# Optimization experiments

Measured on AMD Instinct MI355X. Metric: run time of the kernel, lower is better.

The kernel has to match this reference:

```python
import jax, jax.numpy as jnp
import numpy as np

# Faithful JAX port of RayObsGraph.forward with T=1.
# torch_geometric GraphConv(x, edge_index) with add-aggregation and no edge
# weights computes: out[i] = lin_root(x[i]) + lin_rel(sum_{(j->i) in E} x[j]),
# where lin_root has no bias and lin_rel has a bias. dense_to_sparse(adj)
# yields an edge (row j -> col i) for every nonzero adj[j, i], so the
# aggregation equals binarize(adj)^T @ x, computed batched here instead of the
# original per-sample Python loop.

GS = 128      # graph_size
OBS = 1024    # obs_dim
H = 256       # gcn_h_size
OUT = 1024    # gcn_outsize
NO = 18       # num_outputs
B = 256

def setup_inputs() -> dict:
    key = jax.random.key(0)
    ks = jax.random.split(key, 16)
    inp = {
        "flat": jax.random.normal(ks[0], (B, OBS), jnp.float32),
        "nodes": jax.random.normal(ks[1], (B, GS, OBS), jnp.float32),
        "num_nodes": jax.random.randint(ks[2], (B,), 0, GS),
        "adj": jax.random.randint(ks[3], (B, GS, GS), 0, 2),
        "seq_lens": jnp.ones((B,), jnp.int32),
        # GraphConv 0: lin_rel (bias) + lin_root (no bias)
        "W0_rel": jax.random.normal(ks[4], (OBS, H), jnp.float32) / np.sqrt(OBS),
        "b0": jnp.zeros((H,), jnp.float32),
        "W0_root": jax.random.normal(ks[5], (OBS, H), jnp.float32) / np.sqrt(OBS),
        # GraphConv 1
        "W1_rel": jax.random.normal(ks[6], (H, OUT), jnp.float32) / np.sqrt(H),
        "b1": jnp.zeros((OUT,), jnp.float32),
        "W1_root": jax.random.normal(ks[7], (H, OUT), jnp.float32) / np.sqrt(H),
        # logit / value branches (SlimFC, activation None)
        "Wl": jax.random.normal(ks[8], (OUT, NO), jnp.float32) / np.sqrt(OUT),
        "bl": jnp.zeros((NO,), jnp.float32),
        "Wv": jax.random.normal(ks[9], (OUT, 1), jnp.float32) / np.sqrt(OUT),
        "bv": jnp.zeros((1,), jnp.float32),
    }
    return inp

def _forward(flat, nodes, adj, num_nodes,
             W0_rel, b0, W0_root, W1_rel, b1, W1_root, Wl, bl, Wv, bv):
    bsz = flat.shape[0]
    bi = jnp.arange(bsz)
    n = num_nodes
    nm1 = jnp.maximum(n - 1, 0)
    has_prev = n > 0

    # dense_to_sparse treats any nonzero entry as an edge (weight unused)
    A = (adj != 0).astype(flat.dtype)                       # [B, GS, GS]
    A = A.at[bi, n, n].set(1.0)
    A = A.at[bi, n, nm1].set(jnp.where(has_prev, 1.0, A[bi, n, nm1]))
    A = A.at[bi, nm1, n].set(jnp.where(has_prev, 1.0, A[bi, nm1, n]))

    # write current observation into node slot num_nodes
    x = nodes.at[bi, n].set(flat)                           # [B, GS, OBS]

    At = jnp.swapaxes(A, 1, 2)                              # message j->i: A^T
    aggr0 = jnp.einsum('bij,bjd->bid', At, x)               # [B, GS, OBS]
    h0 = jax.nn.relu(aggr0 @ W0_rel + b0 + x @ W0_root)     # [B, GS, H]
    aggr1 = jnp.einsum('bij,bjd->bid', At, h0)              # [B, GS, H]
    h1 = jax.nn.relu(aggr1 @ W1_rel + b1 + h0 @ W1_root)    # [B, GS, OUT]

    node_out = h1[bi, n]                                    # [B, OUT]
    logits = node_out @ Wl + bl                             # [B, NO]
    values = (node_out @ Wv + bv).squeeze(-1)               # [B]
    return logits, values

def reference(flat, nodes, num_nodes, adj, seq_lens,
              W0_rel, b0, W0_root, W1_rel, b1, W1_root, Wl, bl, Wv, bv):
    # seq_lens only determines B = len(seq_lens); T = flat.shape[0] // B = 1
    del seq_lens
    return _forward(flat, nodes, adj, num_nodes,
                    W0_rel, b0, W0_root, W1_rel, b1, W1_root, Wl, bl, Wv, bv)
```

## Files before the change

### kernel.cpp

```cpp
#include <hip/hip_runtime.h>
#include <hip/hip_bf16.h>
#include <cstdint>
#include <cstddef>

#define GS     128
#define OBS    1024
#define HSZ    256
#define OUTSZ  1024
#define NOUT   18
#define BATCH  256

typedef short  short8  __attribute__((ext_vector_type(8)));
typedef float  f32x4   __attribute__((ext_vector_type(4)));

__device__ __forceinline__ uint32_t f2bf_bits(float f) {
  uint32_t u = __builtin_bit_cast(uint32_t, f);
  return (u + 0x7fffu + ((u >> 16) & 1u)) >> 16;
}
__device__ __forceinline__ float bf_bits2f(uint32_t b) {
  return __builtin_bit_cast(float, b << 16);
}
__device__ __forceinline__ uint4 cvt8s(const float4 a, const float4 b) {
  float v[8] = {a.x, a.y, a.z, a.w, b.x, b.y, b.z, b.w};
  uint32_t h[8];
#pragma unroll
  for (int e = 0; e < 8; ++e) h[e] = f2bf_bits(v[e]);
  return make_uint4(h[0] | (h[1] << 16), h[2] | (h[3] << 16),
                    h[4] | (h[5] << 16), h[6] | (h[7] << 16));
}

__global__ __launch_bounds__(256) void prep_kernel(
    const float* __restrict__ W0_rel, const float* __restrict__ W0_root,
    ushort* __restrict__ WtP, const float* __restrict__ Wl,
    const float* __restrict__ Wv, float* __restrict__ WlT,
    const float* __restrict__ W1_rel, const float* __restrict__ W1_root,
    ushort* __restrict__ W1bf)
{
  __shared__ float T[64][65];
  const int blk = blockIdx.x;
  const int t = threadIdx.x;
  if (blk < 128) {
    const int k0 = (blk & 15) * 64;
    const int n0 = (blk >> 4) * 64;
    for (int idx = t; idx < 4096; idx += 256) {
      const int r = idx >> 6, c = idx & 63;
      const int n = n0 + c;
      T[r][c] = (n < HSZ) ? W0_rel[(size_t)(k0 + r) * HSZ + n]
                          : W0_root[(size_t)(k0 + r) * HSZ + (n - HSZ)];
    }
    __syncthreads();
    for (int idx = t; idx < 4096; idx += 256) {
      const int r = idx >> 6, c = idx & 63;
      const int kk = k0 + c;
      WtP[((size_t)((kk >> 5) * 512 + n0 + r)) * 32 + (kk & 31)] =
          (ushort)f2bf_bits(T[c][r]);
    }
  } else if (blk < 132) {
    const int o = (blk - 128) * 256 + t;
#pragma unroll
    for (int c = 0; c < NOUT; ++c)
      WlT[(size_t)c * OUTSZ + o] = Wl[(size_t)o * NOUT + c];
    WlT[(size_t)18 * OUTSZ + o] = Wv[o];
  } else {
    const int base = (blk - 132) * 16384;
    for (int it = 0; it < 64; ++it) {
      const int idx = base + it * 256 + t;
      const int k = idx >> 10, o = idx & 1023;
      const float v = (k < HSZ) ? W1_rel[(size_t)k * OUTSZ + o]
                                : W1_root[(size_t)(k - HSZ) * OUTSZ + o];
      W1bf[idx] = (ushort)f2bf_bits(v);
    }
  }
}

__global__ __launch_bounds__(256, 1) void mega_kernel(
    const float* __restrict__ flat, const float* __restrict__ nodes,
    const int* __restrict__ num_nodes, const int* __restrict__ adj,
    const float* __restrict__ b0, const ushort* __restrict__ WtP,
    const ushort* __restrict__ W1bf, const float* __restrict__ b1,
    const float* __restrict__ WlT, const float* __restrict__ bl,
    const float* __restrict__ bv, float* __restrict__ out)
{
  __shared__ ushort   Ys[256][264];
  __shared__ ushort   As[128][40];
  __shared__ uint32_t rm[128][4];
  __shared__ uint32_t cmL[128][4];
  __shared__ float    a1s[256];
  __shared__ float    rns[256];
  __shared__ float    pl[19][4];

  const int b  = blockIdx.x;
  const int nb = num_nodes[b];
  const int t  = threadIdx.x;
  const int wv = t >> 6, lane = t & 63;
  const int ln = lane & 15, q = lane >> 4;

#pragma unroll 4
  for (int i = 0; i < 32; ++i) {
    const int k = wv * 32 + i;
    const int* arow = adj + ((size_t)b * GS + k) * GS;
    const unsigned long long m0 = __ballot(arow[lane] != 0);
    const unsigned long long m1 = __ballot(arow[64 + lane] != 0);
    if (lane == 0) {
      rm[k][0] = (uint32_t)m0; rm[k][1] = (uint32_t)(m0 >> 32);
      rm[k][2] = (uint32_t)m1; rm[k][3] = (uint32_t)(m1 >> 32);
    }
  }
  __syncthreads();
  if (t < 128) {
    uint32_t c0 = 0, c1 = 0, c2 = 0, c3 = 0;
    const int w = t >> 5, sh = t & 31;
#pragma unroll 8
    for (int k = 0; k < 128; ++k) {
      const uint32_t bit = (rm[k][w] >> sh) & 1u;
      if (k < 32)      c0 |= bit << k;
      else if (k < 64) c1 |= bit << (k - 32);
      else if (k < 96) c2 |= bit << (k - 64);
      else             c3 |= bit << (k - 96);
    }
    cmL[t][0] = c0; cmL[t][1] = c1; cmL[t][2] = c2; cmL[t][3] = c3;
  }
  __syncthreads();
  if (t == 0) {
    cmL[nb][nb >> 5] |= 1u << (nb & 31);
    if (nb > 0) {
      cmL[nb - 1][nb >> 5] |= 1u << (nb & 31);
      cmL[nb][(nb - 1) >> 5] |= 1u << ((nb - 1) & 31);
    }
  }

  const int arow2 = t >> 1;
  const int akb   = (t & 1) * 16;
  const float* xsrc = ((arow2 == nb) ? (flat + (size_t)b * OBS)
                                     : (nodes + ((size_t)b * GS + arow2) * OBS)) + akb;
  const ushort* bptr = WtP + ((size_t)(wv * 128 + ln)) * 32 + q * 8;

  f32x4 acc[8][8] = {};

  float4 pa0 = *(const float4*)(xsrc);
  float4 pa1 = *(const float4*)(xsrc + 4);
  float4 pa2 = *(const float4*)(xsrc + 8);
  float4 pa3 = *(const float4*)(xsrc + 12);
  float4 qa0, qa1, qa2, qa3;

  short8 bha[8], bhb[8];
#pragma unroll
  for (int jj = 0; jj < 8; ++jj)
    bha[jj] = *(const short8*)(bptr + jj * 512);

  for (int ks = 0; ks < 32; ks += 2) {
    *(uint4*)&As[arow2][akb]     = cvt8s(pa0, pa1);
    *(uint4*)&As[arow2][akb + 8] = cvt8s(pa2, pa3);
    {
      const int kn = (ks + 1) * 32;
      qa0 = *(const float4*)(xsrc + kn);
      qa1 = *(const float4*)(xsrc + kn + 4);
      qa2 = *(const float4*)(xsrc + kn + 8);
      qa3 = *(const float4*)(xsrc + kn + 12);
    }
    __syncthreads();
    {
      const ushort* bp = bptr + (size_t)(ks + 1) * 16384;
#pragma unroll
      for (int jj = 0; jj < 8; ++jj)
        bhb[jj] = *(const short8*)(bp + jj * 512);
    }
    short8 ah[8];
#pragma unroll
    for (int ii = 0; ii < 8; ++ii)
      ah[ii] = *(const short8*)&As[ii * 16 + ln][q * 8];
#pragma unroll
    for (int jj = 0; jj < 8; ++jj)
#pragma unroll
      for (int ii = 0; ii < 8; ++ii)
        acc[jj][ii] = __builtin_amdgcn_mfma_f32_16x16x32_bf16(
            bha[jj], ah[ii], acc[jj][ii], 0, 0, 0);
    __syncthreads();

    *(uint4*)&As[arow2][akb]     = cvt8s(qa0, qa1);
    *(uint4*)&As[arow2][akb + 8] = cvt8s(qa2, qa3);
    if (ks + 2 < 32) {
      const int kn = (ks + 2) * 32;
      pa0 = *(const float4*)(xsrc + kn);
      pa1 = *(const float4*)(xsrc + kn + 4);
      pa2 = *(const float4*)(xsrc + kn + 8);
      pa3 = *(const float4*)(xsrc + kn + 12);
    }
    __syncthreads();
    if (ks + 2 < 32) {
      const ushort* bp = bptr + (size_t)(ks + 2) * 16384;
#pragma unroll
      for (int jj = 0; jj < 8; ++jj)
        bha[jj] = *(const short8*)(bp + jj * 512);
    }
#pragma unroll
    for (int ii = 0; ii < 8; ++ii)
      ah[ii] = *(const short8*)&As[ii * 16 + ln][q * 8];
#pragma unroll
    for (int jj = 0; jj < 8; ++jj)
#pragma unroll
      for (int ii = 0; ii < 8; ++ii)
        acc[jj][ii] = __builtin_amdgcn_mfma_f32_16x16x32_bf16(
            bhb[jj], ah[ii], acc[jj][ii], 0, 0, 0);
    __syncthreads();
  }

#pragma unroll
  for (int jj = 0; jj < 8; ++jj) {
    const int cat = wv * 128 + jj * 16 + q * 4;
    const int h   = cat & 255;
    const int kof = (cat < 256) ? 0 : 128;
#pragma unroll
    for (int ii = 0; ii < 8; ++ii) {
      const int kk = kof + ii * 16 + ln;
#pragma unroll
      for (int r = 0; r < 4; ++r)
        Ys[h + r][kk] = (ushort)f2bf_bits(acc[jj][ii][r]);
    }
  }
  __syncthreads();

  f32x4 acc2[8][4] = {};
  for (int ks = 0; ks < 4; ++ks) {
    short8 bf[4];
#pragma unroll
    for (int ht = 0; ht < 4; ++ht)
      bf[ht] = *(const short8*)&Ys[wv * 64 + ht * 16 + ln][ks * 32 + q * 8];
#pragma unroll
    for (int jt = 0; jt < 8; ++jt) {
      const uint32_t w = cmL[jt * 16 + ln][ks];
      const uint32_t byte = (w >> (q * 8)) & 0xFFu;
      short8 af;
#pragma unroll
      for (int i = 0; i < 8; ++i)
        af[i] = (short)(((byte >> i) & 1u) ? 0x3F80 : 0);
#pragma unroll
      for (int ht = 0; ht < 4; ++ht)
        acc2[jt][ht] = __builtin_amdgcn_mfma_f32_16x16x32_bf16(
            af, bf[ht], acc2[jt][ht], 0, 0, 0);
    }
  }

  const uint32_t S0 = cmL[nb][0], S1 = cmL[nb][1],
                 S2 = cmL[nb][2], S3 = cmL[nb][3];
  float bb[4];
#pragma unroll
  for (int ht = 0; ht < 4; ++ht) bb[ht] = b0[wv * 64 + ht * 16 + ln];

  float asum[4] = {0.f, 0.f, 0.f, 0.f};
#pragma unroll
  for (int jt = 0; jt < 8; ++jt)
#pragma unroll
    for (int r = 0; r < 4; ++r) {
      const int j = jt * 16 + q * 4 + r;
      const uint32_t Sw = (j < 32) ? S0 : (j < 64) ? S1 : (j < 96) ? S2 : S3;
      const bool sj = (Sw >> (j & 31)) & 1u;
      const bool isn = (j == nb);
#pragma unroll
      for (int ht = 0; ht < 4; ++ht) {
        const int hl = wv * 64 + ht * 16 + ln;
        const float yroot = bf_bits2f(Ys[hl][128 + j]);
        const float v = fmaxf(bb[ht] + yroot + acc2[jt][ht][r], 0.f);
        if (sj) asum[ht] += v;
        if (isn) rns[hl] = v;
      }
    }
#pragma unroll
  for (int ht = 0; ht < 4; ++ht) {
    float s = asum[ht];
    s += __shfl_down(s, 32);
    s += __shfl_down(s, 16);
    if (q == 0) a1s[wv * 64 + ht * 16 + ln] = s;
  }
  __syncthreads();

  const int o4 = t * 4;
  float4 a = *(const float4*)&b1[o4];
  const ushort* wp = W1bf + o4;
#pragma unroll 8
  for (int k = 0; k < 256; ++k) {
    const ushort4 w4 = *(const ushort4*)(wp + (size_t)k * OUTSZ);
    const float s = a1s[k];
    a.x = fmaf(s, bf_bits2f(w4.x), a.x);
    a.y = fmaf(s, bf_bits2f(w4.y), a.y);
    a.z = fmaf(s, bf_bits2f(w4.z), a.z);
    a.w = fmaf(s, bf_bits2f(w4.w), a.w);
  }
#pragma unroll 8
  for (int k = 0; k < 256; ++k) {
    const ushort4 w4 = *(const ushort4*)(wp + (size_t)(256 + k) * OUTSZ);
    const float s = rns[k];
    a.x = fmaf(s, bf_bits2f(w4.x), a.x);
    a.y = fmaf(s, bf_bits2f(w4.y), a.y);
    a.z = fmaf(s, bf_bits2f(w4.z), a.z);
    a.w = fmaf(s, bf_bits2f(w4.w), a.w);
  }
  a.x = fmaxf(a.x, 0.f); a.y = fmaxf(a.y, 0.f);
  a.z = fmaxf(a.z, 0.f); a.w = fmaxf(a.w, 0.f);

  float p[19];
#pragma unroll
  for (int c = 0; c < 19; ++c) {
    const float4 w = *(const float4*)&WlT[(size_t)c * OUTSZ + o4];
    p[c] = a.x * w.x + a.y * w.y + a.z * w.z + a.w * w.w;
  }
#pragma unroll
  for (int c = 0; c < 19; ++c) {
    float v = p[c];
    v += __shfl_down(v, 32); v += __shfl_down(v, 16);
    v += __shfl_down(v, 8);  v += __shfl_down(v, 4);
    v += __shfl_down(v, 2);  v += __shfl_down(v, 1);
    if (lane == 0) pl[c][wv] = v;
  }
  __syncthreads();
  if (t < 19) {
    const float s = pl[t][0] + pl[t][1] + pl[t][2] + pl[t][3];
    if (t < NOUT) out[(size_t)b * NOUT + t] = s + bl[t];
    else          out[(size_t)BATCH * NOUT + b] = s + bv[0];
  }
}

extern "C" void kernel_launch(void* const* d_in, const int* in_sizes, int n_in,
                              void* d_out, int out_size, void* d_ws, size_t ws_size,
                              hipStream_t stream)
{
  const float* flat      = (const float*)d_in[0];
  const float* nodes     = (const float*)d_in[1];
  const int*   num_nodes = (const int*)  d_in[2];
  const int*   adj       = (const int*)  d_in[3];
  const float* W0_rel    = (const float*)d_in[5];
  const float* b0        = (const float*)d_in[6];
  const float* W0_root   = (const float*)d_in[7];
  const float* W1_rel    = (const float*)d_in[8];
  const float* b1        = (const float*)d_in[9];
  const float* W1_root   = (const float*)d_in[10];
  const float* Wl        = (const float*)d_in[11];
  const float* bl        = (const float*)d_in[12];
  const float* Wv        = (const float*)d_in[13];
  const float* bv        = (const float*)d_in[14];
  float* out = (float*)d_out;

  char* ws = (char*)d_ws;
  ushort* WtP  = (ushort*)ws;  ws += (size_t)512 * OBS * 2;
  float*  WlT  = (float*)ws;   ws += (size_t)19 * OUTSZ * 4;
  ushort* W1bf = (ushort*)ws;  ws += (size_t)512 * OUTSZ * 2;

  prep_kernel<<<164, 256, 0, stream>>>(
      W0_rel, W0_root, WtP, Wl, Wv, WlT, W1_rel, W1_root, W1bf);
  mega_kernel<<<BATCH, 256, 0, stream>>>(
      flat, nodes, num_nodes, adj, b0, WtP, W1bf, b1, WlT, bl, bv, out);
}
```

Baseline: 317.4 us.

## Use 512 threads per block with double-buffered A tile and split W1 GEMV

Doubles the mega_kernel block to 8 waves so each wave owns half as many output columns in the first GEMM, cutting accumulator registers from 64 to 32 tiles. The A staging tile becomes double-buffered, giving one barrier per k-step and prefetching B fragments one step ahead. The final W1 matvec is split across two thread halves with an LDS partial-sum reduction, and the prep kernel writes transposed weights as 16-byte vectors. The intent is more latency hiding from the extra waves; the cost is a larger shared buffer that aliases Ys, As and the partial sums, and launch_bounds(512,2) may not fit with about 135KB of LDS per block.

```diff
diff --git a/kernel.cpp b/kernel.cpp
--- a/kernel.cpp
+++ b/kernel.cpp
@@ -49,11 +49,16 @@
                           : W0_root[(size_t)(k0 + r) * HSZ + (n - HSZ)];
     }
     __syncthreads();
-    for (int idx = t; idx < 4096; idx += 256) {
-      const int r = idx >> 6, c = idx & 63;
-      const int kk = k0 + c;
-      WtP[((size_t)((kk >> 5) * 512 + n0 + r)) * 32 + (kk & 31)] =
-          (ushort)f2bf_bits(T[c][r]);
+    for (int idx = t; idx < 512; idx += 256) {
+      const int nl = idx >> 3;
+      const int kc = idx & 7;
+      uint32_t h[8];
+#pragma unroll
+      for (int e = 0; e < 8; ++e) h[e] = f2bf_bits(T[kc * 8 + e][nl]);
+      const int kg = k0 + kc * 8;
+      const uint4 w = make_uint4(h[0] | (h[1] << 16), h[2] | (h[3] << 16),
+                                 h[4] | (h[5] << 16), h[6] | (h[7] << 16));
+      *(uint4*)&WtP[((size_t)((kg >> 5) * 512 + n0 + nl)) * 32 + (kg & 31)] = w;
     }
   } else if (blk < 132) {
     const int o = (blk - 128) * 256 + t;
@@ -73,7 +78,7 @@
   }
 }
 
-__global__ __launch_bounds__(256, 1) void mega_kernel(
+__global__ __launch_bounds__(512, 2) void mega_kernel(
     const float* __restrict__ flat, const float* __restrict__ nodes,
     const int* __restrict__ num_nodes, const int* __restrict__ adj,
     const float* __restrict__ b0, const ushort* __restrict__ WtP,
@@ -81,8 +86,10 @@
     const float* __restrict__ WlT, const float* __restrict__ bl,
     const float* __restrict__ bv, float* __restrict__ out)
 {
-  __shared__ ushort   Ys[256][264];
-  __shared__ ushort   As[128][40];
+  __shared__ alignas(16) char smem[135168];
+  ushort (*Ys)[264]     = (ushort (*)[264])smem;
+  ushort (*As)[128][40] = (ushort (*)[128][40])smem;
+  float  (*part)[4]     = (float  (*)[4])smem;
   __shared__ uint32_t rm[128][4];
   __shared__ uint32_t cmL[128][4];
   __shared__ float    a1s[256];
@@ -96,8 +103,8 @@
   const int ln = lane & 15, q = lane >> 4;
 
 #pragma unroll 4
-  for (int i = 0; i < 32; ++i) {
-    const int k = wv * 32 + i;
+  for (int i = 0; i < 16; ++i) {
+    const int k = wv * 16 + i;
     const int* arow = adj + ((size_t)b * GS + k) * GS;
     const unsigned long long m0 = __ballot(arow[lane] != 0);
     const unsigned long long m1 = __ballot(arow[64 + lane] != 0);
@@ -129,85 +136,91 @@
     }
   }
 
-  const int arow2 = t >> 1;
-  const int akb   = (t & 1) * 16;
+  const int arow2 = t >> 2;
+  const int akb   = (t & 3) * 8;
   const float* xsrc = ((arow2 == nb) ? (flat + (size_t)b * OBS)
                                      : (nodes + ((size_t)b * GS + arow2) * OBS)) + akb;
-  const ushort* bptr = WtP + ((size_t)(wv * 128 + ln)) * 32 + q * 8;
-
-  f32x4 acc[8][8] = {};
-
-  float4 pa0 = *(const float4*)(xsrc);
-  float4 pa1 = *(const float4*)(xsrc + 4);
-  float4 pa2 = *(const float4*)(xsrc + 8);
-  float4 pa3 = *(const float4*)(xsrc + 12);
-  float4 qa0, qa1, qa2, qa3;
-
-  short8 bha[8], bhb[8];
-#pragma unroll
-  for (int jj = 0; jj < 8; ++jj)
-    bha[jj] = *(const short8*)(bptr + jj * 512);
-
-  for (int ks = 0; ks < 32; ks += 2) {
-    *(uint4*)&As[arow2][akb]     = cvt8s(pa0, pa1);
-    *(uint4*)&As[arow2][akb + 8] = cvt8s(pa2, pa3);
+  const ushort* bptr = WtP + ((size_t)(wv * 64 + ln)) * 32 + q * 8;
+
+  f32x4 acc[4][8] = {};
+
+  {
+    const float4 c0 = *(const float4*)(xsrc);
+    const float4 c1 = *(const float4*)(xsrc + 4);
+    *(uint4*)&As[0][arow2][akb] = cvt8s(c0, c1);
+  }
+  float4 gA = *(const float4*)(xsrc + 32);
+  float4 gB = *(const float4*)(xsrc + 36);
+  short8 bc0 = *(const short8*)(bptr);
+  short8 bc1 = *(const short8*)(bptr + 512);
+  short8 bc2 = *(const short8*)(bptr + 1024);
+  short8 bc3 = *(const short8*)(bptr + 1536);
+  __syncthreads();
+
+  for (int s = 0; s < 32; s += 2) {
     {
-      const int kn = (ks + 1) * 32;
-      qa0 = *(const float4*)(xsrc + kn);
-      qa1 = *(const float4*)(xsrc + kn + 4);
-      qa2 = *(const float4*)(xsrc + kn + 8);
-      qa3 = *(const float4*)(xsrc + kn + 12);
-    }
-    __syncthreads();
+      float4 fA = {}, fB = {};
+      if (s + 2 < 32) {
+        fA = *(const float4*)(xsrc + (s + 2) * 32);
+        fB = *(const float4*)(xsrc + (s + 2) * 32 + 4);
+      }
+      const ushort* bp = bptr + (size_t)(s + 1) * 16384;
+      const short8 bn0 = *(const short8*)(bp);
+      const short8 bn1 = *(const short8*)(bp + 512);
+      const short8 bn2 = *(const short8*)(bp + 1024);
+      const short8 bn3 = *(const short8*)(bp + 1536);
+      short8 ah[8];
+#pragma unroll
+      for (int ii = 0; ii < 8; ++ii)
+        ah[ii] = *(const short8*)&As[0][ii * 16 + ln][q * 8];
+#pragma unroll
+      for (int ii = 0; ii < 8; ++ii) {
+        acc[0][ii] = __builtin_amdgcn_mfma_f32_16x16x32_bf16(bc0, ah[ii], acc[0][ii], 0, 0, 0);
+        acc[1][ii] = __builtin_amdgcn_mfma_f32_16x16x32_bf16(bc1, ah[ii], acc[1][ii], 0, 0, 0);
+        acc[2][ii] = __builtin_amdgcn_mfma_f32_16x16x32_bf16(bc2, ah[ii], acc[2][ii], 0, 0, 0);
+        acc[3][ii] = __builtin_amdgcn_mfma_f32_16x16x32_bf16(bc3, ah[ii], acc[3][ii], 0, 0, 0);
+      }
+      *(uint4*)&As[1][arow2][akb] = cvt8s(gA, gB);
+      gA = fA; gB = fB;
+      bc0 = bn0; bc1 = bn1; bc2 = bn2; bc3 = bn3;
+      __syncthreads();
+    }
     {
-      const ushort* bp = bptr + (size_t)(ks + 1) * 16384;
-#pragma unroll
-      for (int jj = 0; jj < 8; ++jj)
-        bhb[jj] = *(const short8*)(bp + jj * 512);
-    }
-    short8 ah[8];
-#pragma unroll
-    for (int ii = 0; ii < 8; ++ii)
-      ah[ii] = *(const short8*)&As[ii * 16 + ln][q * 8];
-#pragma unroll
-    for (int jj = 0; jj < 8; ++jj)
+      float4 fA = {}, fB = {};
+      if (s + 3 < 32) {
+        fA = *(const float4*)(xsrc + (s + 3) * 32);
+        fB = *(const float4*)(xsrc + (s + 3) * 32 + 4);
+      }
+      short8 bn0 = {}, bn1 = {}, bn2 = {}, bn3 = {};
+      if (s + 2 < 32) {
+        const ushort* bp = bptr + (size_t)(s + 2) * 16384;
+        bn0 = *(const short8*)(bp);
+        bn1 = *(const short8*)(bp + 512);
+        bn2 = *(const short8*)(bp + 1024);
+        bn3 = *(const short8*)(bp + 1536);
+      }
+      short8 ah[8];
 #pragma unroll
       for (int ii = 0; ii < 8; ++ii)
-        acc[jj][ii] = __builtin_amdgcn_mfma_f32_16x16x32_bf16(
-            bha[jj], ah[ii], acc[jj][ii], 0, 0, 0);
-    __syncthreads();
-
-    *(uint4*)&As[arow2][akb]     = cvt8s(qa0, qa1);
-    *(uint4*)&As[arow2][akb + 8] = cvt8s(qa2, qa3);
-    if (ks + 2 < 32) {
-      const int kn = (ks + 2) * 32;
-      pa0 = *(const float4*)(xsrc + kn);
-      pa1 = *(const float4*)(xsrc + kn + 4);
-      pa2 = *(const float4*)(xsrc + kn + 8);
-      pa3 = *(const float4*)(xsrc + kn + 12);
-    }
-    __syncthreads();
-    if (ks + 2 < 32) {
-      const ushort* bp = bptr + (size_t)(ks + 2) * 16384;
-#pragma unroll
-      for (int jj = 0; jj < 8; ++jj)
-        bha[jj] = *(const short8*)(bp + jj * 512);
-    }
-#pragma unroll
-    for (int ii = 0; ii < 8; ++ii)
-      ah[ii] = *(const short8*)&As[ii * 16 + ln][q * 8];
-#pragma unroll
-    for (int jj = 0; jj < 8; ++jj)
-#pragma unroll
-      for (int ii = 0; ii < 8; ++ii)
-        acc[jj][ii] = __builtin_amdgcn_mfma_f32_16x16x32_bf16(
-            bhb[jj], ah[ii], acc[jj][ii], 0, 0, 0);
-    __syncthreads();
-  }
-
-#pragma unroll
-  for (int jj = 0; jj < 8; ++jj) {
-    const int cat = wv * 128 + jj * 16 + q * 4;
+        ah[ii] = *(const short8*)&As[1][ii * 16 + ln][q * 8];
+#pragma unroll
+      for (int ii = 0; ii < 8; ++ii) {
+        acc[0][ii] = __builtin_amdgcn_mfma_f32_16x16x32_bf16(bc0, ah[ii], acc[0][ii], 0, 0, 0);
+        acc[1][ii] = __builtin_amdgcn_mfma_f32_16x16x32_bf16(bc1, ah[ii], acc[1][ii], 0, 0, 0);
+        acc[2][ii] = __builtin_amdgcn_mfma_f32_16x16x32_bf16(bc2, ah[ii], acc[2][ii], 0, 0, 0);
+        acc[3][ii] = __builtin_amdgcn_mfma_f32_16x16x32_bf16(bc3, ah[ii], acc[3][ii], 0, 0, 0);
+      }
+      if (s + 2 < 32)
+        *(uint4*)&As[0][arow2][akb] = cvt8s(gA, gB);
+      gA = fA; gB = fB;
+      bc0 = bn0; bc1 = bn1; bc2 = bn2; bc3 = bn3;
+      __syncthreads();
+    }
+  }
+
+#pragma unroll
+  for (int jj = 0; jj < 4; ++jj) {
+    const int cat = wv * 64 + jj * 16 + q * 4;
     const int h   = cat & 255;
     const int kof = (cat < 256) ? 0 : 128;
 #pragma unroll
@@ -220,34 +233,30 @@
   }
   __syncthreads();
 
-  f32x4 acc2[8][4] = {};
+  f32x4 acc2[8][2] = {};
+#pragma unroll
   for (int ks = 0; ks < 4; ++ks) {
-    short8 bf[4];
-#pragma unroll
-    for (int ht = 0; ht < 4; ++ht)
-      bf[ht] = *(const short8*)&Ys[wv * 64 + ht * 16 + ln][ks * 32 + q * 8];
+    const short8 bf0 = *(const short8*)&Ys[wv * 32 + ln][ks * 32 + q * 8];
+    const short8 bf1 = *(const short8*)&Ys[wv * 32 + 16 + ln][ks * 32 + q * 8];
 #pragma unroll
     for (int jt = 0; jt < 8; ++jt) {
       const uint32_t w = cmL[jt * 16 + ln][ks];
-      const uint32_t byte = (w >> (q * 8)) & 0xFFu;
+      const uint32_t byte_ = (w >> (q * 8)) & 0xFFu;
       short8 af;
 #pragma unroll
       for (int i = 0; i < 8; ++i)
-        af[i] = (short)(((byte >> i) & 1u) ? 0x3F80 : 0);
-#pragma unroll
-      for (int ht = 0; ht < 4; ++ht)
-        acc2[jt][ht] = __builtin_amdgcn_mfma_f32_16x16x32_bf16(
-            af, bf[ht], acc2[jt][ht], 0, 0, 0);
+        af[i] = (short)(((byte_ >> i) & 1u) ? 0x3F80 : 0);
+      acc2[jt][0] = __builtin_amdgcn_mfma_f32_16x16x32_bf16(af, bf0, acc2[jt][0], 0, 0, 0);
+      acc2[jt][1] = __builtin_amdgcn_mfma_f32_16x16x32_bf16(af, bf1, acc2[jt][1], 0, 0, 0);
     }
   }
 
   const uint32_t S0 = cmL[nb][0], S1 = cmL[nb][1],
                  S2 = cmL[nb][2], S3 = cmL[nb][3];
-  float bb[4];
-#pragma unroll
-  for (int ht = 0; ht < 4; ++ht) bb[ht] = b0[wv * 64 + ht * 16 + ln];
-
-  float asum[4] = {0.f, 0.f, 0.f, 0.f};
+  const float bb0 = b0[wv * 32 + ln];
+  const float bb1 = b0[wv * 32 + 16 + ln];
+
+  float asum0 = 0.f, asum1 = 0.f;
 #pragma unroll
   for (int jt = 0; jt < 8; ++jt)
 #pragma unroll
@@ -256,61 +265,68 @@
       const uint32_t Sw = (j < 32) ? S0 : (j < 64) ? S1 : (j < 96) ? S2 : S3;
       const bool sj = (Sw >> (j & 31)) & 1u;
       const bool isn = (j == nb);
-#pragma unroll
-      for (int ht = 0; ht < 4; ++ht) {
-        const int hl = wv * 64 + ht * 16 + ln;
+      {
+        const int hl = wv * 32 + ln;
         const float yroot = bf_bits2f(Ys[hl][128 + j]);
-        const float v = fmaxf(bb[ht] + yroot + acc2[jt][ht][r], 0.f);
-        if (sj) asum[ht] += v;
+        const float v = fmaxf(bb0 + yroot + acc2[jt][0][r], 0.f);
+        if (sj) asum0 += v;
         if (isn) rns[hl] = v;
       }
-    }
-#pragma unroll
-  for (int ht = 0; ht < 4; ++ht) {
-    float s = asum[ht];
-    s += __shfl_down(s, 32);
-    s += __shfl_down(s, 16);
-    if (q == 0) a1s[wv * 64 + ht * 16 + ln] = s;
-  }
-  __syncthreads();
-
-  const int o4 = t * 4;
-  float4 a = *(const float4*)&b1[o4];
-  const ushort* wp = W1bf + o4;
+      {
+        const int hl = wv * 32 + 16 + ln;
+        const float yroot = bf_bits2f(Ys[hl][128 + j]);
+        const float v = fmaxf(bb1 + yroot + acc2[jt][1][r], 0.f);
+        if (sj) asum1 += v;
+        if (isn) rns[hl] = v;
+      }
+    }
+  asum0 += __shfl_down(asum0, 32);
+  asum0 += __shfl_down(asum0, 16);
+  asum1 += __shfl_down(asum1, 32);
+  asum1 += __shfl_down(asum1, 16);
+  if (q == 0) {
+    a1s[wv * 32 + ln]      = asum0;
+    a1s[wv * 32 + 16 + ln] = asum1;
+  }
+  __syncthreads();
+
+  const int oh = t >> 8;
+  const int o4 = (t & 255) * 4;
+  float4 a = make_float4(0.f, 0.f, 0.f, 0.f);
+  if (oh == 0) a = *(const float4*)&b1[o4];
+  const ushort* wp = W1bf + (size_t)oh * 256 * OUTSZ + o4;
+  const float* sv = oh ? rns : a1s;
 #pragma unroll 8
   for (int k = 0; k < 256; ++k) {
     const ushort4 w4 = *(const ushort4*)(wp + (size_t)k * OUTSZ);
-    const float s = a1s[k];
+    const float s = sv[k];
     a.x = fmaf(s, bf_bits2f(w4.x), a.x);
     a.y = fmaf(s, bf_bits2f(w4.y), a.y);
     a.z = fmaf(s, bf_bits2f(w4.z), a.z);
     a.w = fmaf(s, bf_bits2f(w4.w), a.w);
   }
-#pragma unroll 8
-  for (int k = 0; k < 256; ++k) {
-    const ushort4 w4 = *(const ushort4*)(wp + (size_t)(256 + k) * OUTSZ);
-    const float s = rns[k];
-    a.x = fmaf(s, bf_bits2f(w4.x), a.x);
-    a.y = fmaf(s, bf_bits2f(w4.y), a.y);
-    a.z = fmaf(s, bf_bits2f(w4.z), a.z);
-    a.w = fmaf(s, bf_bits2f(w4.w), a.w);
-  }
-  a.x = fmaxf(a.x, 0.f); a.y = fmaxf(a.y, 0.f);
-  a.z = fmaxf(a.z, 0.f); a.w = fmaxf(a.w, 0.f);
-
-  float p[19];
-#pragma unroll
-  for (int c = 0; c < 19; ++c) {
-    const float4 w = *(const float4*)&WlT[(size_t)c * OUTSZ + o4];
-    p[c] = a.x * w.x + a.y * w.y + a.z * w.z + a.w * w.w;
-  }
-#pragma unroll
-  for (int c = 0; c < 19; ++c) {
-    float v = p[c];
-    v += __shfl_down(v, 32); v += __shfl_down(v, 16);
-    v += __shfl_down(v, 8);  v += __shfl_down(v, 4);
-    v += __shfl_down(v, 2);  v += __shfl_down(v, 1);
-    if (lane == 0) pl[c][wv] = v;
+  if (oh == 1) *(float4*)&part[t & 255][0] = a;
+  __syncthreads();
+  if (oh == 0) {
+    const float4 pb = *(const float4*)&part[t & 255][0];
+    a.x = fmaxf(a.x + pb.x, 0.f);
+    a.y = fmaxf(a.y + pb.y, 0.f);
+    a.z = fmaxf(a.z + pb.z, 0.f);
+    a.w = fmaxf(a.w + pb.w, 0.f);
+    float p[19];
+#pragma unroll
+    for (int c = 0; c < 19; ++c) {
+      const float4 w = *(const float4*)&WlT[(size_t)c * OUTSZ + o4];
+      p[c] = a.x * w.x + a.y * w.y + a.z * w.z + a.w * w.w;
+    }
+#pragma unroll
+    for (int c = 0; c < 19; ++c) {
+      float v = p[c];
+      v += __shfl_down(v, 32); v += __shfl_down(v, 16);
+      v += __shfl_down(v, 8);  v += __shfl_down(v, 4);
+      v += __shfl_down(v, 2);  v += __shfl_down(v, 1);
+      if (lane == 0) pl[c][wv] = v;
+    }
   }
   __syncthreads();
   if (t < 19) {
@@ -347,6 +363,6 @@
 
   prep_kernel<<<164, 256, 0, stream>>>(
       W0_rel, W0_root, WtP, Wl, Wv, WlT, W1_rel, W1_root, W1bf);
-  mega_kernel<<<BATCH, 256, 0, stream>>>(
+  mega_kernel<<<BATCH, 512, 0, stream>>>(
       flat, nodes, num_nodes, adj, b0, WtP, W1bf, b1, WlT, bl, bv, out);
 }
```

New measurement: 299.1 us. -5.8%, faster.
